# Performance work log

Measured on AMD Instinct MI355X. Metric: run time of the kernel, lower is better.

## Reference

```python
import jax, jax.numpy as jnp
import numpy as np

N = 1024; D = 128; H = 128; FF = 2048; NHEAD = 4; VOCAB = 32000; EPS = 1e-5


def _ln(x, s, b):
    m = x.mean(-1, keepdims=True)
    v = ((x - m) ** 2).mean(-1, keepdims=True)
    return (x - m) / jnp.sqrt(v + EPS) * s + b


def _mha(x, qkv_w, qkv_b, ow, ob):
    n, d = x.shape
    hd = d // NHEAD
    qkv = x @ qkv_w.T + qkv_b  # (n, 3d)
    q, k, v = [t.reshape(n, NHEAD, hd).transpose(1, 0, 2) for t in jnp.split(qkv, 3, axis=-1)]
    scores = jnp.einsum('hqd,hkd->hqk', q, k) / np.float32(np.sqrt(hd))
    attn = jax.nn.softmax(scores, axis=-1)
    o = jnp.einsum('hqk,hkd->hqd', attn, v).transpose(1, 0, 2).reshape(n, d)
    return o @ ow.T + ob


def setup_inputs() -> dict:
    key = jax.random.key(0)
    ks = jax.random.split(key, 10)
    s = 0.02
    p = lambda k, shape: (jax.random.normal(k, shape, jnp.float32) * s)
    return {
        'inputs': jax.random.randint(ks[0], (N,), 0, VOCAB),
        'emb': p(ks[1], (VOCAB, D)),
        'qkv_w': p(ks[2], (2, 3 * D, D)), 'qkv_b': jnp.zeros((2, 3 * D), jnp.float32),
        'attn_out_w': p(ks[3], (2, D, D)), 'attn_out_b': jnp.zeros((2, D), jnp.float32),
        'ln1_s': jnp.ones((2, D), jnp.float32), 'ln1_b': jnp.zeros((2, D), jnp.float32),
        'ln2_s': jnp.ones((2, D), jnp.float32), 'ln2_b': jnp.zeros((2, D), jnp.float32),
        'ff1_w': p(ks[4], (2, FF, D)), 'ff1_b': jnp.zeros((2, FF), jnp.float32),
        'ff2_w': p(ks[5], (2, D, FF)), 'ff2_b': jnp.zeros((2, D), jnp.float32),
        'w1': p(ks[6], (H, 2 * D)), 'b1': jnp.zeros((H,), jnp.float32),
        'w2': p(ks[7], (1, H)), 'b2': jnp.zeros((1,), jnp.float32),
    }


def reference(inputs, emb, qkv_w, qkv_b, attn_out_w, attn_out_b, ln1_s, ln1_b,
              ln2_s, ln2_b, ff1_w, ff1_b, ff2_w, ff2_b, w1, b1, w2, b2):
    x = emb[inputs]  # (n, d)
    for l in range(2):  # post-norm TransformerEncoderLayer (torch default)
        x = _ln(x + _mha(x, qkv_w[l], qkv_b[l], attn_out_w[l], attn_out_b[l]), ln1_s[l], ln1_b[l])
        ff = jax.nn.relu(x @ ff1_w[l].T + ff1_b[l]) @ ff2_w[l].T + ff2_b[l]
        x = _ln(x + ff, ln2_s[l], ln2_b[l])
    # pair MLP: concat(e_i, e_j) @ W1.T == e_i @ W1_left.T + e_j @ W1_right.T
    a = x @ w1[:, :D].T  # (n, H)
    b = x @ w1[:, D:].T  # (n, H)
    h = jax.nn.relu(a[:, None, :] + b[None, :, :] + b1)  # (n, n, H)
    return (h @ w2.T + b2)[..., 0]  # (n, n)
```

## Files before the change

### kernel.cpp

```cpp
#include <hip/hip_runtime.h>
#include <math.h>

#define QK_SCALE 0.17677669529663687f

typedef __attribute__((ext_vector_type(8))) short bf16x8;
typedef __attribute__((ext_vector_type(4))) float f32x4;

__device__ __forceinline__ unsigned short f2bf(float f) {
    unsigned u = __float_as_uint(f);
    u = u + 0x7FFFu + ((u >> 16) & 1u);
    return (unsigned short)(u >> 16);
}

__global__ void pre_kernel(const int* __restrict__ ids, const float* __restrict__ emb,
                           const float* __restrict__ qkv_w, const float* __restrict__ ow,
                           const float* __restrict__ ff1_w, const float* __restrict__ ff2_w,
                           const float* __restrict__ w1,
                           unsigned short* __restrict__ qkv_wb, unsigned short* __restrict__ owb,
                           unsigned short* __restrict__ ff1b, unsigned short* __restrict__ ff2b,
                           unsigned short* __restrict__ w1L, unsigned short* __restrict__ w1R,
                           float* __restrict__ x, unsigned short* __restrict__ xb) {
    const int blk = blockIdx.x, t = threadIdx.x;
    if (blk < 4608) {
        int i = blk * 256 + t;
        if (i < 98304)       qkv_wb[i] = f2bf(qkv_w[i]);
        else if (i < 131072) owb[i - 98304] = f2bf(ow[i - 98304]);
        else if (i < 655360) ff1b[i - 131072] = f2bf(ff1_w[i - 131072]);
        else                 ff2b[i - 655360] = f2bf(ff2_w[i - 655360]);
    } else if (blk < 4736) {
        int i = (blk - 4608) * 256 + t;
        int h = i >> 8, c = i & 255;
        float v = w1[i];
        if (c < 128) w1L[h * 128 + c] = f2bf(v);
        else         w1R[h * 128 + (c - 128)] = f2bf(v);
    } else {
        int u = (blk - 4736) * 256 + t;
        int i = u >> 5, d4 = (u & 31) * 4;
        float4 v = *(const float4*)&emb[(size_t)ids[i] * 128 + d4];
        *(float4*)&x[i * 128 + d4] = v;
        ushort4 bv;
        bv.x = f2bf(v.x); bv.y = f2bf(v.y); bv.z = f2bf(v.z); bv.w = f2bf(v.w);
        *(ushort4*)&xb[i * 128 + d4] = bv;
    }
}

__global__ __launch_bounds__(256) void qkv_gemm(const unsigned short* __restrict__ Xb,
                                                const unsigned short* __restrict__ Wb,
                                                const float* __restrict__ bias,
                                                float* __restrict__ C) {
    const int lane = threadIdx.x & 63, w = threadIdx.x >> 6;
    const int m0 = blockIdx.y * 64 + w * 16;
    const int n0 = blockIdx.x * 64;
    const int r16 = lane & 15, kh = lane >> 4;
    f32x4 acc[4] = {{0.f,0.f,0.f,0.f},{0.f,0.f,0.f,0.f},{0.f,0.f,0.f,0.f},{0.f,0.f,0.f,0.f}};
    const unsigned short* Ap = Xb + (size_t)(m0 + r16) * 128 + kh * 8;
    const unsigned short* Bp = Wb + (size_t)(n0 + r16) * 128 + kh * 8;
#pragma unroll
    for (int k0 = 0; k0 < 128; k0 += 32) {
        bf16x8 a = *(const bf16x8*)(Ap + k0);
#pragma unroll
        for (int nt = 0; nt < 4; ++nt) {
            bf16x8 b = *(const bf16x8*)(Bp + (size_t)nt * 16 * 128 + k0);
            acc[nt] = __builtin_amdgcn_mfma_f32_16x16x32_bf16(a, b, acc[nt], 0, 0, 0);
        }
    }
#pragma unroll
    for (int nt = 0; nt < 4; ++nt) {
        int col = n0 + nt * 16 + r16;
        float bv = bias[col];
#pragma unroll
        for (int r = 0; r < 4; ++r) {
            int row = m0 + kh * 4 + r;
            C[(size_t)row * 384 + col] = acc[nt][r] + bv;
        }
    }
}

__global__ __launch_bounds__(256) void attn_flash(const float* __restrict__ qkv,
                                                  unsigned short* __restrict__ attn_ob) {
    const int h = blockIdx.y;
    const int q0 = blockIdx.x * 16;
    const int t = threadIdx.x;
    const int qi = t & 15;
    const int g = t >> 4;
    __shared__ float Kt[64][36];
    __shared__ float Vt[64][36];
    __shared__ float opart[16][16][36];
    __shared__ float rsum[16][17];

    float qreg[32];
    const float* Qp = qkv + (size_t)(q0 + qi) * 384 + h * 32;
#pragma unroll
    for (int d4 = 0; d4 < 8; ++d4) {
        float4 v = *(const float4*)(Qp + d4 * 4);
        qreg[d4 * 4 + 0] = v.x * QK_SCALE; qreg[d4 * 4 + 1] = v.y * QK_SCALE;
        qreg[d4 * 4 + 2] = v.z * QK_SCALE; qreg[d4 * 4 + 3] = v.w * QK_SCALE;
    }
    float opar[32] = {};
    float psum = 0.f;

    for (int j0 = 0; j0 < 1024; j0 += 64) {
        __syncthreads();
#pragma unroll
        for (int u = 0; u < 2; ++u) {
            int uu = t + u * 256;
            int r = uu >> 3, dq = (uu & 7) * 4;
            const float* src = qkv + (size_t)(j0 + r) * 384 + 128 + h * 32 + dq;
            float4 kv = *(const float4*)src;
            float4 vv = *(const float4*)(src + 128);
            *(float4*)&Kt[r][dq] = kv;
            *(float4*)&Vt[r][dq] = vv;
        }
        __syncthreads();
#pragma unroll
        for (int jj = 0; jj < 4; ++jj) {
            const int jl = g * 4 + jj;
            float s = 0.f;
#pragma unroll
            for (int d4 = 0; d4 < 8; ++d4) {
                float4 kv = *(const float4*)&Kt[jl][d4 * 4];
                s += qreg[d4 * 4 + 0] * kv.x + qreg[d4 * 4 + 1] * kv.y
                   + qreg[d4 * 4 + 2] * kv.z + qreg[d4 * 4 + 3] * kv.w;
            }
            float p = __expf(s);
            psum += p;
#pragma unroll
            for (int d4 = 0; d4 < 8; ++d4) {
                float4 vv = *(const float4*)&Vt[jl][d4 * 4];
                opar[d4 * 4 + 0] += p * vv.x; opar[d4 * 4 + 1] += p * vv.y;
                opar[d4 * 4 + 2] += p * vv.z; opar[d4 * 4 + 3] += p * vv.w;
            }
        }
    }

#pragma unroll
    for (int d4 = 0; d4 < 8; ++d4)
        *(float4*)&opart[g][qi][d4 * 4] = make_float4(opar[d4 * 4 + 0], opar[d4 * 4 + 1],
                                                      opar[d4 * 4 + 2], opar[d4 * 4 + 3]);
    rsum[qi][g] = psum;
    __syncthreads();
    {
        const int qi2 = t & 15;
        const int d0 = (t >> 4) * 2;
        float ssum = 0.f;
#pragma unroll
        for (int gg = 0; gg < 16; ++gg) ssum += rsum[qi2][gg];
        float inv = 1.0f / ssum;
        float o0 = 0.f, o1 = 0.f;
#pragma unroll
        for (int gg = 0; gg < 16; ++gg) {
            o0 += opart[gg][qi2][d0];
            o1 += opart[gg][qi2][d0 + 1];
        }
        unsigned short* dst = attn_ob + (size_t)(q0 + qi2) * 128 + h * 32 + d0;
        dst[0] = f2bf(o0 * inv);
        dst[1] = f2bf(o1 * inv);
    }
}

__global__ __launch_bounds__(256) void mega_mlp(
    const unsigned short* __restrict__ attn_ob, const unsigned short* __restrict__ owb,
    const float* __restrict__ ob, const float* __restrict__ x_res,
    const float* __restrict__ ln1_s, const float* __restrict__ ln1_b,
    const unsigned short* __restrict__ f1w, const float* __restrict__ f1bias,
    const unsigned short* __restrict__ f2w, const float* __restrict__ f2bias,
    const float* __restrict__ ln2_s, const float* __restrict__ ln2_b,
    float* __restrict__ x_out, unsigned short* __restrict__ xb_out,
    const unsigned short* __restrict__ w1L, const unsigned short* __restrict__ w1R,
    float* __restrict__ pab, int do_pair) {
    __shared__ unsigned short fflds[16 * 2048];
    __shared__ float ylds[16][132];
    __shared__ unsigned short xlds[16 * 128];
    const int t = threadIdx.x, lane = t & 63, w = t >> 6;
    const int r16 = lane & 15, kh = lane >> 4;
    const int r0 = blockIdx.x * 16;

    {
        const int n0 = w * 32;
        f32x4 acc[2] = {{0.f,0.f,0.f,0.f},{0.f,0.f,0.f,0.f}};
        const unsigned short* Ap = attn_ob + (size_t)(r0 + r16) * 128 + kh * 8;
        const unsigned short* Bp = owb + (size_t)(n0 + r16) * 128 + kh * 8;
#pragma unroll
        for (int k0 = 0; k0 < 128; k0 += 32) {
            bf16x8 a = *(const bf16x8*)(Ap + k0);
#pragma unroll
            for (int nt = 0; nt < 2; ++nt) {
                bf16x8 b = *(const bf16x8*)(Bp + (size_t)nt * 16 * 128 + k0);
                acc[nt] = __builtin_amdgcn_mfma_f32_16x16x32_bf16(a, b, acc[nt], 0, 0, 0);
            }
        }
#pragma unroll
        for (int nt = 0; nt < 2; ++nt) {
            int col = n0 + nt * 16 + r16;
            float bv = ob[col];
#pragma unroll
            for (int r = 0; r < 4; ++r) {
                int rl = kh * 4 + r;
                ylds[rl][col] = acc[nt][r] + bv + x_res[(size_t)(r0 + rl) * 128 + col];
            }
        }
    }
    __syncthreads();

    {
        int row = t >> 4, c0 = (t & 15) * 8;
        float4 va = *(float4*)&ylds[row][c0];
        float4 vb = *(float4*)&ylds[row][c0 + 4];
        float s1 = va.x + va.y + va.z + va.w + vb.x + vb.y + vb.z + vb.w;
        float s2 = va.x*va.x + va.y*va.y + va.z*va.z + va.w*va.w
                 + vb.x*vb.x + vb.y*vb.y + vb.z*vb.z + vb.w*vb.w;
#pragma unroll
        for (int o = 1; o < 16; o <<= 1) { s1 += __shfl_xor(s1, o); s2 += __shfl_xor(s2, o); }
        float mean = s1 * (1.0f / 128.0f);
        float inv = rsqrtf(s2 * (1.0f / 128.0f) - mean * mean + 1e-5f);
        int sw = (row & 7) << 3;
        unsigned short hb[8];
        float rv[8] = {va.x, va.y, va.z, va.w, vb.x, vb.y, vb.z, vb.w};
#pragma unroll
        for (int j = 0; j < 8; ++j) {
            int c = c0 + j;
            float r = (rv[j] - mean) * inv * ln1_s[c] + ln1_b[c];
            ylds[row][c] = r;
            hb[j] = f2bf(r);
        }
        *(ushort4*)&xlds[row * 128 + (c0 ^ sw)] = make_ushort4(hb[0], hb[1], hb[2], hb[3]);
        *(ushort4*)&xlds[row * 128 + ((c0 + 4) ^ sw)] = make_ushort4(hb[4], hb[5], hb[6], hb[7]);
    }
    __syncthreads();

    {
        bf16x8 a[4];
        int swa = (r16 & 7) << 3;
#pragma unroll
        for (int i = 0; i < 4; ++i)
            a[i] = *(const bf16x8*)&xlds[r16 * 128 + ((i * 32 + kh * 8) ^ swa)];
#pragma unroll
        for (int chunk = 0; chunk < 2; ++chunk) {
            int cbase = w * 512 + chunk * 256;
            f32x4 acc[16];
#pragma unroll
            for (int nt = 0; nt < 16; ++nt) acc[nt] = (f32x4){0.f, 0.f, 0.f, 0.f};
#pragma unroll
            for (int nt = 0; nt < 16; ++nt) {
                const unsigned short* Bp = f1w + (size_t)(cbase + nt * 16 + r16) * 128 + kh * 8;
#pragma unroll
                for (int k0 = 0; k0 < 4; ++k0) {
                    bf16x8 b = *(const bf16x8*)(Bp + k0 * 32);
                    acc[nt] = __builtin_amdgcn_mfma_f32_16x16x32_bf16(a[k0], b, acc[nt], 0, 0, 0);
                }
            }
#pragma unroll
            for (int nt = 0; nt < 16; ++nt) {
                int col = cbase + nt * 16 + r16;
                float bv = f1bias[col];
#pragma unroll
                for (int r = 0; r < 4; ++r) {
                    int row = kh * 4 + r;
                    float v = fmaxf(acc[nt][r] + bv, 0.f);
                    fflds[row * 2048 + (col ^ ((row & 7) << 3))] = f2bf(v);
                }
            }
        }
    }
    __syncthreads();

    {
        const int n0 = w * 32;
        f32x4 acc[2] = {{0.f,0.f,0.f,0.f},{0.f,0.f,0.f,0.f}};
        int swa = (r16 & 7) << 3;
#pragma unroll 8
        for (int ks = 0; ks < 64; ++ks) {
            int kk = ks * 32 + kh * 8;
            bf16x8 a = *(const bf16x8*)&fflds[r16 * 2048 + (kk ^ swa)];
#pragma unroll
            for (int nt = 0; nt < 2; ++nt) {
                bf16x8 b = *(const bf16x8*)(f2w + (size_t)(n0 + nt * 16 + r16) * 2048 + kk);
                acc[nt] = __builtin_amdgcn_mfma_f32_16x16x32_bf16(a, b, acc[nt], 0, 0, 0);
            }
        }
#pragma unroll
        for (int nt = 0; nt < 2; ++nt) {
            int col = n0 + nt * 16 + r16;
            float bv = f2bias[col];
#pragma unroll
            for (int r = 0; r < 4; ++r) {
                int rl = kh * 4 + r;
                ylds[rl][col] = acc[nt][r] + bv + ylds[rl][col];
            }
        }
    }
    __syncthreads();

    {
        int row = t >> 4, c0 = (t & 15) * 8;
        float4 va = *(float4*)&ylds[row][c0];
        float4 vb = *(float4*)&ylds[row][c0 + 4];
        float s1 = va.x + va.y + va.z + va.w + vb.x + vb.y + vb.z + vb.w;
        float s2 = va.x*va.x + va.y*va.y + va.z*va.z + va.w*va.w
                 + vb.x*vb.x + vb.y*vb.y + vb.z*vb.z + vb.w*vb.w;
#pragma unroll
        for (int o = 1; o < 16; o <<= 1) { s1 += __shfl_xor(s1, o); s2 += __shfl_xor(s2, o); }
        float mean = s1 * (1.0f / 128.0f);
        float inv = rsqrtf(s2 * (1.0f / 128.0f) - mean * mean + 1e-5f);
        int sw = (row & 7) << 3;
        float rv[8] = {va.x, va.y, va.z, va.w, vb.x, vb.y, vb.z, vb.w};
        float ro[8];
        unsigned short hb[8];
#pragma unroll
        for (int j = 0; j < 8; ++j) {
            int c = c0 + j;
            ro[j] = (rv[j] - mean) * inv * ln2_s[c] + ln2_b[c];
            hb[j] = f2bf(ro[j]);
        }
        size_t gbase = (size_t)(r0 + row) * 128 + c0;
        *(float4*)&x_out[gbase]     = make_float4(ro[0], ro[1], ro[2], ro[3]);
        *(float4*)&x_out[gbase + 4] = make_float4(ro[4], ro[5], ro[6], ro[7]);
        *(ushort4*)&xb_out[gbase]     = make_ushort4(hb[0], hb[1], hb[2], hb[3]);
        *(ushort4*)&xb_out[gbase + 4] = make_ushort4(hb[4], hb[5], hb[6], hb[7]);
        *(ushort4*)&xlds[row * 128 + (c0 ^ sw)]       = make_ushort4(hb[0], hb[1], hb[2], hb[3]);
        *(ushort4*)&xlds[row * 128 + ((c0 + 4) ^ sw)] = make_ushort4(hb[4], hb[5], hb[6], hb[7]);
    }
    if (!do_pair) return;
    __syncthreads();

    {
        bf16x8 a[4];
        int swa = (r16 & 7) << 3;
#pragma unroll
        for (int i = 0; i < 4; ++i)
            a[i] = *(const bf16x8*)&xlds[r16 * 128 + ((i * 32 + kh * 8) ^ swa)];
        const int n0 = w * 32;
        f32x4 accA[2] = {{0.f,0.f,0.f,0.f},{0.f,0.f,0.f,0.f}};
        f32x4 accB[2] = {{0.f,0.f,0.f,0.f},{0.f,0.f,0.f,0.f}};
#pragma unroll
        for (int k0 = 0; k0 < 4; ++k0) {
#pragma unroll
            for (int nt = 0; nt < 2; ++nt) {
                const unsigned short* BA = w1L + (size_t)(n0 + nt * 16 + r16) * 128 + kh * 8 + k0 * 32;
                const unsigned short* BB = w1R + (size_t)(n0 + nt * 16 + r16) * 128 + kh * 8 + k0 * 32;
                accA[nt] = __builtin_amdgcn_mfma_f32_16x16x32_bf16(a[k0], *(const bf16x8*)BA, accA[nt], 0, 0, 0);
                accB[nt] = __builtin_amdgcn_mfma_f32_16x16x32_bf16(a[k0], *(const bf16x8*)BB, accB[nt], 0, 0, 0);
            }
        }
#pragma unroll
        for (int nt = 0; nt < 2; ++nt) {
            int col = n0 + nt * 16 + r16;
#pragma unroll
            for (int r = 0; r < 4; ++r) {
                int row = r0 + kh * 4 + r;
                pab[(size_t)row * 128 + col] = accA[nt][r];
                pab[131072 + (size_t)row * 128 + col] = accB[nt][r];
            }
        }
    }
}

__global__ __launch_bounds__(256) void pair_kernel(const float* __restrict__ A,
                                                   const float* __restrict__ B,
                                                   const float* __restrict__ b1,
                                                   const float* __restrict__ w2,
                                                   const float* __restrict__ b2p,
                                                   float* __restrict__ outp) {
    __shared__ float As[32][132];
    __shared__ float Bs[32][132];
    __shared__ float w2s[128];
    const int t = threadIdx.x;
    const int tx = t & 15, ty = t >> 4;
    const int i0 = blockIdx.y * 32, j0 = blockIdx.x * 32;
    for (int u = t; u < 1024; u += 256) {
        int r = u >> 5, kq = (u & 31) * 4;
        float4 av = *(const float4*)&A[(size_t)(i0 + r) * 128 + kq];
        float4 bb1 = *(const float4*)&b1[kq];
        av.x += bb1.x; av.y += bb1.y; av.z += bb1.z; av.w += bb1.w;
        *(float4*)&As[r][kq] = av;
        *(float4*)&Bs[r][kq] = *(const float4*)&B[(size_t)(j0 + r) * 128 + kq];
    }
    if (t < 32) *(float4*)&w2s[t * 4] = *(const float4*)&w2[t * 4];
    __syncthreads();
    float a00 = 0.f, a01 = 0.f, a10 = 0.f, a11 = 0.f;
#pragma unroll 4
    for (int k4 = 0; k4 < 32; ++k4) {
        float4 x0 = *(const float4*)&As[ty][k4 * 4];
        float4 x1 = *(const float4*)&As[ty + 16][k4 * 4];
        float4 y0 = *(const float4*)&Bs[tx][k4 * 4];
        float4 y1 = *(const float4*)&Bs[tx + 16][k4 * 4];
        float4 w = *(const float4*)&w2s[k4 * 4];
        a00 += fmaxf(x0.x + y0.x, 0.f) * w.x + fmaxf(x0.y + y0.y, 0.f) * w.y
             + fmaxf(x0.z + y0.z, 0.f) * w.z + fmaxf(x0.w + y0.w, 0.f) * w.w;
        a01 += fmaxf(x0.x + y1.x, 0.f) * w.x + fmaxf(x0.y + y1.y, 0.f) * w.y
             + fmaxf(x0.z + y1.z, 0.f) * w.z + fmaxf(x0.w + y1.w, 0.f) * w.w;
        a10 += fmaxf(x1.x + y0.x, 0.f) * w.x + fmaxf(x1.y + y0.y, 0.f) * w.y
             + fmaxf(x1.z + y0.z, 0.f) * w.z + fmaxf(x1.w + y0.w, 0.f) * w.w;
        a11 += fmaxf(x1.x + y1.x, 0.f) * w.x + fmaxf(x1.y + y1.y, 0.f) * w.y
             + fmaxf(x1.z + y1.z, 0.f) * w.z + fmaxf(x1.w + y1.w, 0.f) * w.w;
    }
    float bb = b2p[0];
    outp[(size_t)(i0 + ty) * 1024 + j0 + tx]            = a00 + bb;
    outp[(size_t)(i0 + ty) * 1024 + j0 + tx + 16]       = a01 + bb;
    outp[(size_t)(i0 + ty + 16) * 1024 + j0 + tx]       = a10 + bb;
    outp[(size_t)(i0 + ty + 16) * 1024 + j0 + tx + 16]  = a11 + bb;
}

extern "C" void kernel_launch(void* const* d_in, const int* in_sizes, int n_in,
                              void* d_out, int out_size, void* d_ws, size_t ws_size,
                              hipStream_t stream) {
    const int*   ids   = (const int*)d_in[0];
    const float* emb   = (const float*)d_in[1];
    const float* qkv_w = (const float*)d_in[2];
    const float* qkv_b = (const float*)d_in[3];
    const float* ow    = (const float*)d_in[4];
    const float* ob    = (const float*)d_in[5];
    const float* ln1_s = (const float*)d_in[6];
    const float* ln1_b = (const float*)d_in[7];
    const float* ln2_s = (const float*)d_in[8];
    const float* ln2_b = (const float*)d_in[9];
    const float* ff1_w = (const float*)d_in[10];
    const float* ff1_b = (const float*)d_in[11];
    const float* ff2_w = (const float*)d_in[12];
    const float* ff2_b = (const float*)d_in[13];
    const float* w1    = (const float*)d_in[14];
    const float* b1    = (const float*)d_in[15];
    const float* w2    = (const float*)d_in[16];
    const float* b2    = (const float*)d_in[17];
    float* out = (float*)d_out;

    float* ws = (float*)d_ws;
    float*          x       = ws;
    unsigned short* xb      = (unsigned short*)(ws + 131072);
    float*          qkvb    = ws + 196608;
    unsigned short* attn_ob = (unsigned short*)(ws + 589824);
    float*          pab     = ws + 655360;
    unsigned short* qkv_wb  = (unsigned short*)(ws + 917504);
    unsigned short* owb     = (unsigned short*)(ws + 966656);
    unsigned short* ff1b    = (unsigned short*)(ws + 983040);
    unsigned short* ff2b    = (unsigned short*)(ws + 1245184);
    unsigned short* w1L     = (unsigned short*)(ws + 1507328);
    unsigned short* w1R     = (unsigned short*)(ws + 1515520);

    pre_kernel<<<4864, 256, 0, stream>>>(ids, emb, qkv_w, ow, ff1_w, ff2_w, w1,
                                         qkv_wb, owb, ff1b, ff2b, w1L, w1R, x, xb);

    for (int l = 0; l < 2; ++l) {
        qkv_gemm<<<dim3(6, 16), 256, 0, stream>>>(xb, qkv_wb + l * 384 * 128,
                                                  qkv_b + l * 384, qkvb);
        attn_flash<<<dim3(64, 4), 256, 0, stream>>>(qkvb, attn_ob);
        mega_mlp<<<64, 256, 0, stream>>>(attn_ob, owb + l * 128 * 128, ob + l * 128, x,
                                         ln1_s + l * 128, ln1_b + l * 128,
                                         ff1b + l * 2048 * 128, ff1_b + l * 2048,
                                         ff2b + l * 128 * 2048, ff2_b + l * 128,
                                         ln2_s + l * 128, ln2_b + l * 128,
                                         x, xb, w1L, w1R, pab, l == 1);
    }

    pair_kernel<<<dim3(32, 32), 256, 0, stream>>>(pab, pab + 131072, b1, w2, b2, out);
}
```

Measured before the change: 276.3 us.

## Move attention to bf16 MFMA and enlarge pair-kernel register tiles

```diff
diff --git a/kernel.cpp b/kernel.cpp
--- a/kernel.cpp
+++ b/kernel.cpp
@@ -47,7 +47,9 @@
 __global__ __launch_bounds__(256) void qkv_gemm(const unsigned short* __restrict__ Xb,
                                                 const unsigned short* __restrict__ Wb,
                                                 const float* __restrict__ bias,
-                                                float* __restrict__ C) {
+                                                unsigned short* __restrict__ qb,
+                                                unsigned short* __restrict__ kb,
+                                                unsigned short* __restrict__ vb) {
     const int lane = threadIdx.x & 63, w = threadIdx.x >> 6;
     const int m0 = blockIdx.y * 64 + w * 16;
     const int n0 = blockIdx.x * 64;
@@ -71,90 +73,95 @@
 #pragma unroll
         for (int r = 0; r < 4; ++r) {
             int row = m0 + kh * 4 + r;
-            C[(size_t)row * 384 + col] = acc[nt][r] + bv;
-        }
-    }
-}
-
-__global__ __launch_bounds__(256) void attn_flash(const float* __restrict__ qkv,
-                                                  unsigned short* __restrict__ attn_ob) {
-    const int h = blockIdx.y;
-    const int q0 = blockIdx.x * 16;
-    const int t = threadIdx.x;
-    const int qi = t & 15;
-    const int g = t >> 4;
-    __shared__ float Kt[64][36];
-    __shared__ float Vt[64][36];
-    __shared__ float opart[16][16][36];
-    __shared__ float rsum[16][17];
-
-    float qreg[32];
-    const float* Qp = qkv + (size_t)(q0 + qi) * 384 + h * 32;
-#pragma unroll
-    for (int d4 = 0; d4 < 8; ++d4) {
-        float4 v = *(const float4*)(Qp + d4 * 4);
-        qreg[d4 * 4 + 0] = v.x * QK_SCALE; qreg[d4 * 4 + 1] = v.y * QK_SCALE;
-        qreg[d4 * 4 + 2] = v.z * QK_SCALE; qreg[d4 * 4 + 3] = v.w * QK_SCALE;
-    }
-    float opar[32] = {};
-    float psum = 0.f;
-
-    for (int j0 = 0; j0 < 1024; j0 += 64) {
+            float v = acc[nt][r] + bv;
+            if (col < 128)      qb[(size_t)row * 128 + col] = f2bf(v * QK_SCALE);
+            else if (col < 256) kb[(size_t)row * 128 + col - 128] = f2bf(v);
+            else                vb[(size_t)row * 128 + col - 256] = f2bf(v);
+        }
+    }
+}
+
+__global__ __launch_bounds__(256) void attn_mfma(const unsigned short* __restrict__ qb,
+                                                 const unsigned short* __restrict__ kb,
+                                                 const unsigned short* __restrict__ vb,
+                                                 unsigned short* __restrict__ attn_ob) {
+    const int h = blockIdx.y, q0 = blockIdx.x * 32;
+    const int t = threadIdx.x, lane = t & 63, w = t >> 6;
+    const int r16 = lane & 15, kh = lane >> 4;
+    const int qsub = w & 1;
+    const int kg = w >> 1;
+    __shared__ __align__(16) unsigned short Qs[32 * 40];
+    __shared__ __align__(16) unsigned short Kt[128 * 40];
+    __shared__ __align__(16) unsigned short Vt[32 * 136];
+    __shared__ __align__(16) unsigned short Ps[32 * 136];
+    __shared__ float psum[32];
+
+    if (t < 128) {
+        int r = t >> 2, c8 = (t & 3) * 8;
+        *(bf16x8*)&Qs[r * 40 + c8] = *(const bf16x8*)&qb[(size_t)(q0 + r) * 128 + h * 32 + c8];
+    }
+    if (t < 32) psum[t] = 0.f;
+    f32x4 oacc = {0.f, 0.f, 0.f, 0.f};
+    __syncthreads();
+
+    for (int kt = 0; kt < 8; ++kt) {
+        const int kbase = kt * 128;
+#pragma unroll
+        for (int rep = 0; rep < 2; ++rep) {
+            int id = rep * 256 + t;
+            int kr = id >> 2, d0 = (id & 3) * 8;
+            *(bf16x8*)&Kt[kr * 40 + d0] =
+                *(const bf16x8*)&kb[(size_t)(kbase + kr) * 128 + h * 32 + d0];
+            bf16x8 vv = *(const bf16x8*)&vb[(size_t)(kbase + kr) * 128 + h * 32 + d0];
+#pragma unroll
+            for (int j = 0; j < 8; ++j)
+                Vt[(d0 + j) * 136 + kr] = (unsigned short)vv[j];
+        }
         __syncthreads();
-#pragma unroll
-        for (int u = 0; u < 2; ++u) {
-            int uu = t + u * 256;
-            int r = uu >> 3, dq = (uu & 7) * 4;
-            const float* src = qkv + (size_t)(j0 + r) * 384 + 128 + h * 32 + dq;
-            float4 kv = *(const float4*)src;
-            float4 vv = *(const float4*)(src + 128);
-            *(float4*)&Kt[r][dq] = kv;
-            *(float4*)&Vt[r][dq] = vv;
+
+        {
+            bf16x8 aq = *(const bf16x8*)&Qs[(qsub * 16 + r16) * 40 + kh * 8];
+            float p[4][4];
+#pragma unroll
+            for (int i = 0; i < 4; ++i) {
+                int ks = kg * 4 + i;
+                bf16x8 bk = *(const bf16x8*)&Kt[(ks * 16 + r16) * 40 + kh * 8];
+                f32x4 s = {0.f, 0.f, 0.f, 0.f};
+                s = __builtin_amdgcn_mfma_f32_16x16x32_bf16(aq, bk, s, 0, 0, 0);
+#pragma unroll
+                for (int r = 0; r < 4; ++r) p[i][r] = __expf(s[r]);
+            }
+#pragma unroll
+            for (int r = 0; r < 4; ++r) {
+                float s = p[0][r] + p[1][r] + p[2][r] + p[3][r];
+                s += __shfl_xor(s, 1); s += __shfl_xor(s, 2);
+                s += __shfl_xor(s, 4); s += __shfl_xor(s, 8);
+                if (r16 == 0) atomicAdd(&psum[qsub * 16 + kh * 4 + r], s);
+            }
+#pragma unroll
+            for (int i = 0; i < 4; ++i) {
+                int ks = kg * 4 + i;
+#pragma unroll
+                for (int r = 0; r < 4; ++r)
+                    Ps[(qsub * 16 + kh * 4 + r) * 136 + ks * 16 + r16] = f2bf(p[i][r]);
+            }
         }
         __syncthreads();
-#pragma unroll
-        for (int jj = 0; jj < 4; ++jj) {
-            const int jl = g * 4 + jj;
-            float s = 0.f;
-#pragma unroll
-            for (int d4 = 0; d4 < 8; ++d4) {
-                float4 kv = *(const float4*)&Kt[jl][d4 * 4];
-                s += qreg[d4 * 4 + 0] * kv.x + qreg[d4 * 4 + 1] * kv.y
-                   + qreg[d4 * 4 + 2] * kv.z + qreg[d4 * 4 + 3] * kv.w;
-            }
-            float p = __expf(s);
-            psum += p;
-#pragma unroll
-            for (int d4 = 0; d4 < 8; ++d4) {
-                float4 vv = *(const float4*)&Vt[jl][d4 * 4];
-                opar[d4 * 4 + 0] += p * vv.x; opar[d4 * 4 + 1] += p * vv.y;
-                opar[d4 * 4 + 2] += p * vv.z; opar[d4 * 4 + 3] += p * vv.w;
-            }
-        }
-    }
-
-#pragma unroll
-    for (int d4 = 0; d4 < 8; ++d4)
-        *(float4*)&opart[g][qi][d4 * 4] = make_float4(opar[d4 * 4 + 0], opar[d4 * 4 + 1],
-                                                      opar[d4 * 4 + 2], opar[d4 * 4 + 3]);
-    rsum[qi][g] = psum;
-    __syncthreads();
-    {
-        const int qi2 = t & 15;
-        const int d0 = (t >> 4) * 2;
-        float ssum = 0.f;
-#pragma unroll
-        for (int gg = 0; gg < 16; ++gg) ssum += rsum[qi2][gg];
-        float inv = 1.0f / ssum;
-        float o0 = 0.f, o1 = 0.f;
-#pragma unroll
-        for (int gg = 0; gg < 16; ++gg) {
-            o0 += opart[gg][qi2][d0];
-            o1 += opart[gg][qi2][d0 + 1];
-        }
-        unsigned short* dst = attn_ob + (size_t)(q0 + qi2) * 128 + h * 32 + d0;
-        dst[0] = f2bf(o0 * inv);
-        dst[1] = f2bf(o1 * inv);
+
+#pragma unroll
+        for (int seg = 0; seg < 4; ++seg) {
+            bf16x8 ap = *(const bf16x8*)&Ps[(qsub * 16 + r16) * 136 + seg * 32 + kh * 8];
+            bf16x8 bv = *(const bf16x8*)&Vt[(kg * 16 + r16) * 136 + seg * 32 + kh * 8];
+            oacc = __builtin_amdgcn_mfma_f32_16x16x32_bf16(ap, bv, oacc, 0, 0, 0);
+        }
+        __syncthreads();
+    }
+
+#pragma unroll
+    for (int r = 0; r < 4; ++r) {
+        int row = qsub * 16 + kh * 4 + r;
+        float o = oacc[r] / psum[row];
+        attn_ob[(size_t)(q0 + row) * 128 + h * 32 + kg * 16 + r16] = f2bf(o);
     }
 }
 
@@ -361,44 +368,57 @@
                                                    const float* __restrict__ w2,
                                                    const float* __restrict__ b2p,
                                                    float* __restrict__ outp) {
-    __shared__ float As[32][132];
-    __shared__ float Bs[32][132];
+    __shared__ float As[64][132];
+    __shared__ float Bst[128][68];
     __shared__ float w2s[128];
     const int t = threadIdx.x;
     const int tx = t & 15, ty = t >> 4;
-    const int i0 = blockIdx.y * 32, j0 = blockIdx.x * 32;
-    for (int u = t; u < 1024; u += 256) {
+    const int i0 = blockIdx.y * 64, j0 = blockIdx.x * 64;
+    for (int u = t; u < 2048; u += 256) {
         int r = u >> 5, kq = (u & 31) * 4;
         float4 av = *(const float4*)&A[(size_t)(i0 + r) * 128 + kq];
         float4 bb1 = *(const float4*)&b1[kq];
         av.x += bb1.x; av.y += bb1.y; av.z += bb1.z; av.w += bb1.w;
         *(float4*)&As[r][kq] = av;
-        *(float4*)&Bs[r][kq] = *(const float4*)&B[(size_t)(j0 + r) * 128 + kq];
+        float4 bv = *(const float4*)&B[(size_t)(j0 + r) * 128 + kq];
+        Bst[kq + 0][r] = bv.x; Bst[kq + 1][r] = bv.y;
+        Bst[kq + 2][r] = bv.z; Bst[kq + 3][r] = bv.w;
     }
     if (t < 32) *(float4*)&w2s[t * 4] = *(const float4*)&w2[t * 4];
     __syncthreads();
-    float a00 = 0.f, a01 = 0.f, a10 = 0.f, a11 = 0.f;
-#pragma unroll 4
+
+    float acc[4][4] = {};
+#pragma unroll 2
     for (int k4 = 0; k4 < 32; ++k4) {
-        float4 x0 = *(const float4*)&As[ty][k4 * 4];
-        float4 x1 = *(const float4*)&As[ty + 16][k4 * 4];
-        float4 y0 = *(const float4*)&Bs[tx][k4 * 4];
-        float4 y1 = *(const float4*)&Bs[tx + 16][k4 * 4];
-        float4 w = *(const float4*)&w2s[k4 * 4];
-        a00 += fmaxf(x0.x + y0.x, 0.f) * w.x + fmaxf(x0.y + y0.y, 0.f) * w.y
-             + fmaxf(x0.z + y0.z, 0.f) * w.z + fmaxf(x0.w + y0.w, 0.f) * w.w;
-        a01 += fmaxf(x0.x + y1.x, 0.f) * w.x + fmaxf(x0.y + y1.y, 0.f) * w.y
-             + fmaxf(x0.z + y1.z, 0.f) * w.z + fmaxf(x0.w + y1.w, 0.f) * w.w;
-        a10 += fmaxf(x1.x + y0.x, 0.f) * w.x + fmaxf(x1.y + y0.y, 0.f) * w.y
-             + fmaxf(x1.z + y0.z, 0.f) * w.z + fmaxf(x1.w + y0.w, 0.f) * w.w;
-        a11 += fmaxf(x1.x + y1.x, 0.f) * w.x + fmaxf(x1.y + y1.y, 0.f) * w.y
-             + fmaxf(x1.z + y1.z, 0.f) * w.z + fmaxf(x1.w + y1.w, 0.f) * w.w;
+        float4 xv0 = *(const float4*)&As[ty * 4 + 0][k4 * 4];
+        float4 xv1 = *(const float4*)&As[ty * 4 + 1][k4 * 4];
+        float4 xv2 = *(const float4*)&As[ty * 4 + 2][k4 * 4];
+        float4 xv3 = *(const float4*)&As[ty * 4 + 3][k4 * 4];
+        float4 wv  = *(const float4*)&w2s[k4 * 4];
+#pragma unroll
+        for (int kk = 0; kk < 4; ++kk) {
+            float4 yv = *(const float4*)&Bst[k4 * 4 + kk][tx * 4];
+            float wk = (kk == 0) ? wv.x : (kk == 1) ? wv.y : (kk == 2) ? wv.z : wv.w;
+            float xs[4] = {
+                (kk == 0) ? xv0.x : (kk == 1) ? xv0.y : (kk == 2) ? xv0.z : xv0.w,
+                (kk == 0) ? xv1.x : (kk == 1) ? xv1.y : (kk == 2) ? xv1.z : xv1.w,
+                (kk == 0) ? xv2.x : (kk == 1) ? xv2.y : (kk == 2) ? xv2.z : xv2.w,
+                (kk == 0) ? xv3.x : (kk == 1) ? xv3.y : (kk == 2) ? xv3.z : xv3.w };
+#pragma unroll
+            for (int i = 0; i < 4; ++i) {
+                acc[i][0] += fmaxf(xs[i] + yv.x, 0.f) * wk;
+                acc[i][1] += fmaxf(xs[i] + yv.y, 0.f) * wk;
+                acc[i][2] += fmaxf(xs[i] + yv.z, 0.f) * wk;
+                acc[i][3] += fmaxf(xs[i] + yv.w, 0.f) * wk;
+            }
+        }
     }
     float bb = b2p[0];
-    outp[(size_t)(i0 + ty) * 1024 + j0 + tx]            = a00 + bb;
-    outp[(size_t)(i0 + ty) * 1024 + j0 + tx + 16]       = a01 + bb;
-    outp[(size_t)(i0 + ty + 16) * 1024 + j0 + tx]       = a10 + bb;
-    outp[(size_t)(i0 + ty + 16) * 1024 + j0 + tx + 16]  = a11 + bb;
+#pragma unroll
+    for (int i = 0; i < 4; ++i) {
+        float4 v = make_float4(acc[i][0] + bb, acc[i][1] + bb, acc[i][2] + bb, acc[i][3] + bb);
+        *(float4*)&outp[(size_t)(i0 + ty * 4 + i) * 1024 + j0 + tx * 4] = v;
+    }
 }
 
 extern "C" void kernel_launch(void* const* d_in, const int* in_sizes, int n_in,
@@ -427,23 +447,25 @@
     float* ws = (float*)d_ws;
     float*          x       = ws;
     unsigned short* xb      = (unsigned short*)(ws + 131072);
-    float*          qkvb    = ws + 196608;
-    unsigned short* attn_ob = (unsigned short*)(ws + 589824);
-    float*          pab     = ws + 655360;
-    unsigned short* qkv_wb  = (unsigned short*)(ws + 917504);
-    unsigned short* owb     = (unsigned short*)(ws + 966656);
-    unsigned short* ff1b    = (unsigned short*)(ws + 983040);
-    unsigned short* ff2b    = (unsigned short*)(ws + 1245184);
-    unsigned short* w1L     = (unsigned short*)(ws + 1507328);
-    unsigned short* w1R     = (unsigned short*)(ws + 1515520);
+    unsigned short* qb      = (unsigned short*)(ws + 196608);
+    unsigned short* kb      = (unsigned short*)(ws + 262144);
+    unsigned short* vb      = (unsigned short*)(ws + 327680);
+    unsigned short* attn_ob = (unsigned short*)(ws + 393216);
+    float*          pab     = ws + 458752;
+    unsigned short* qkv_wb  = (unsigned short*)(ws + 720896);
+    unsigned short* owb     = (unsigned short*)(ws + 770048);
+    unsigned short* ff1b    = (unsigned short*)(ws + 786432);
+    unsigned short* ff2b    = (unsigned short*)(ws + 1048576);
+    unsigned short* w1L     = (unsigned short*)(ws + 1310720);
+    unsigned short* w1R     = (unsigned short*)(ws + 1318912);
 
     pre_kernel<<<4864, 256, 0, stream>>>(ids, emb, qkv_w, ow, ff1_w, ff2_w, w1,
                                          qkv_wb, owb, ff1b, ff2b, w1L, w1R, x, xb);
 
     for (int l = 0; l < 2; ++l) {
         qkv_gemm<<<dim3(6, 16), 256, 0, stream>>>(xb, qkv_wb + l * 384 * 128,
-                                                  qkv_b + l * 384, qkvb);
-        attn_flash<<<dim3(64, 4), 256, 0, stream>>>(qkvb, attn_ob);
+                                                  qkv_b + l * 384, qb, kb, vb);
+        attn_mfma<<<dim3(32, 4), 256, 0, stream>>>(qb, kb, vb, attn_ob);
         mega_mlp<<<64, 256, 0, stream>>>(attn_ob, owb + l * 128 * 128, ob + l * 128, x,
                                          ln1_s + l * 128, ln1_b + l * 128,
                                          ff1b + l * 2048 * 128, ff1_b + l * 2048,
@@ -452,5 +474,5 @@
                                          x, xb, w1L, w1R, pab, l == 1);
     }
 
-    pair_kernel<<<dim3(32, 32), 256, 0, stream>>>(pab, pab + 131072, b1, w2, b2, out);
-}
+    pair_kernel<<<dim3(16, 16), 256, 0, stream>>>(pab, pab + 131072, b1, w2, b2, out);
+}
```

New measurement: 241.0 us. 12.8% less time.
